# Performance work log

Hardware: AMD Instinct MI355X
Metric: run time of the kernel (lower is better)

The kernel has to match this reference:

```python
import jax, jax.numpy as jnp
import numpy as np

B, S, H = 8, 1024, 768      # batch, seq_len, encoder hidden
T, D = 9, 64                # output_type_size, att_dim
NEG = -1e12                 # masked_fill value from original code


def rope_tables(seq_len, dim):
    # theta_i = 10000^(-2i/dim), repeat_interleave(2) -> [t0,t0,t1,t1,...]
    pos = jnp.arange(seq_len, dtype=jnp.float32)[:, None]           # [S,1]
    theta = jnp.power(10000.0, -2.0 * jnp.arange(dim // 2, dtype=jnp.float32) / dim)
    theta = jnp.repeat(theta, 2)                                     # [D]
    ang = pos * theta[None, :]                                       # [S,D]
    return jnp.cos(ang), jnp.sin(ang)


def setup_inputs() -> dict:
    key = jax.random.key(0)
    k1, k2 = jax.random.split(key)
    hidden = jax.random.normal(k1, (B, S, H), dtype=jnp.float32)
    attention_mask = jnp.ones((B, S), dtype=jnp.int32)
    # xavier_normal-ish init for dense weight [2*T*D, H], zero bias
    fan = H + T * D * 2
    W = jax.random.normal(k2, (T * D * 2, H), dtype=jnp.float32) * (2.0 / fan) ** 0.5
    b = jnp.zeros((T * D * 2,), dtype=jnp.float32)
    return {"hidden": hidden, "attention_mask": attention_mask, "W": W, "b": b}


def reference(hidden, attention_mask, W, b):
    Bsz, Sl, _ = hidden.shape
    out = hidden @ W.T + b                          # [B,S,2*T*D]
    out = out.reshape(Bsz, Sl, T, D, 2)
    q = out[..., 0].transpose(0, 2, 1, 3)           # [B,T,S,D]
    k = out[..., 1].transpose(0, 2, 1, 3)           # [B,T,S,D]

    cos, sin = rope_tables(Sl, D)                   # [S,D] each

    def rot(x):
        # faithful to original: cat([-x[...,1::2], x[...,::2]], -1), NOT interleaved
        x2 = jnp.concatenate([-x[..., 1::2], x[..., ::2]], axis=-1)
        return x * cos + x2 * sin

    q, k = rot(q), rot(k)

    logits = jnp.einsum('btmd,btnd->btmn', q, k)    # [B,T,S,S]

    am = attention_mask.astype(bool)
    pad = am[:, None, :, None] & am[:, None, None, :]   # [B,1,S,S]
    triu = jnp.triu(jnp.ones((Sl, Sl), dtype=bool))     # spans i<=j
    return jnp.where(pad & triu, logits, NEG)
```

## Files before the change

kernel.cpp:

```cpp
#include <hip/hip_runtime.h>

#define S_LEN 1024
#define HID   768
#define T_SZ  9
#define NEG_VAL (-1e12f)

typedef __bf16 bf16x8 __attribute__((ext_vector_type(8)));
typedef float  f32x4  __attribute__((ext_vector_type(4)));
typedef short  short8 __attribute__((ext_vector_type(8)));
typedef short  short4v __attribute__((ext_vector_type(4)));
typedef float  float4v __attribute__((ext_vector_type(4)));

__device__ __forceinline__ unsigned short f2bf(float f) {
    unsigned int u = __builtin_bit_cast(unsigned int, f);
    u += 0x7FFFu + ((u >> 16) & 1u);
    return (unsigned short)(u >> 16);
}

__device__ __forceinline__ void gload_lds16(const void* g, void* l) {
    __builtin_amdgcn_global_load_lds(
        (const __attribute__((address_space(1))) unsigned int*)g,
        (__attribute__((address_space(3))) unsigned int*)l,
        16, 0, 0);
}

__global__ __launch_bounds__(256) void k_convert(const float* __restrict__ src,
                                                 unsigned short* __restrict__ dst,
                                                 int n8) {
    int i = blockIdx.x * 256 + threadIdx.x;
    if (i >= n8) return;
    float4v a = *((const float4v*)src + (size_t)i * 2);
    float4v b = *((const float4v*)src + (size_t)i * 2 + 1);
    short8 o;
    o[0] = (short)f2bf(a[0]); o[1] = (short)f2bf(a[1]);
    o[2] = (short)f2bf(a[2]); o[3] = (short)f2bf(a[3]);
    o[4] = (short)f2bf(b[0]); o[5] = (short)f2bf(b[1]);
    o[6] = (short)f2bf(b[2]); o[7] = (short)f2bf(b[3]);
    *(short8*)(dst + (size_t)i * 8) = o;
}

__global__ void k_tables(float* __restrict__ cosT, float* __restrict__ sinT) {
    int idx = blockIdx.x * 256 + threadIdx.x;
    int s = idx >> 6;
    int d = idx & 63;
    float theta = exp2f(-13.2877123795f * (float)(d >> 1) * (1.0f / 32.0f));
    float ang = (float)s * theta;
    float sv, cv;
    sincosf(ang, &sv, &cv);
    cosT[idx] = cv;
    sinT[idx] = sv;
}

__global__ __launch_bounds__(256) void k_proj_rope(
    const unsigned short* __restrict__ hidB,
    const unsigned short* __restrict__ wB,
    const float* __restrict__ bias,
    const float* __restrict__ cosT,
    const float* __restrict__ sinT,
    unsigned short* __restrict__ qout,
    unsigned short* __restrict__ kout)
{
    __shared__ union __align__(16) {
        struct { unsigned short A[128 * 64]; unsigned short B[128 * 64]; } st;
        unsigned short Tr[128 * 136];
    } sm;

    int tid = threadIdx.x;
    int mt = blockIdx.x / 9;
    int t  = blockIdx.x % 9;
    int m0 = mt * 128;
    int n0 = t * 128;

    int lane = tid & 63;
    int wave = tid >> 6;
    int lr = lane & 15;
    int lq = lane >> 4;
    int wrow = wave * 32;

    float bv[8];
    #pragma unroll
    for (int fn = 0; fn < 8; ++fn) bv[fn] = bias[n0 + fn * 16 + lr];

    const unsigned short* aSrc[4];
    const unsigned short* bSrc[4];
    #pragma unroll
    for (int it = 0; it < 4; ++it) {
        int gsi = (wave * 4 + it) * 64 + lane;
        int r = gsi >> 3;
        int sw = gsi & 7;
        int seg8 = (sw ^ (r & 7)) << 3;
        aSrc[it] = hidB + (size_t)(m0 + r) * HID + seg8;
        bSrc[it] = wB  + (size_t)(n0 + r) * HID + seg8;
    }

    f32x4 acc[2][8];
    #pragma unroll
    for (int i = 0; i < 2; ++i)
        #pragma unroll
        for (int j = 0; j < 8; ++j) acc[i][j] = (f32x4){0.f, 0.f, 0.f, 0.f};

    for (int kk = 0; kk < HID / 64; ++kk) {
        __syncthreads();
        #pragma unroll
        for (int it = 0; it < 4; ++it) {
            gload_lds16(aSrc[it] + kk * 64, &sm.st.A[(wave * 4 + it) * 512]);
            gload_lds16(bSrc[it] + kk * 64, &sm.st.B[(wave * 4 + it) * 512]);
        }
        __syncthreads();
        #pragma unroll
        for (int kb = 0; kb < 2; ++kb) {
            bf16x8 af[2];
            #pragma unroll
            for (int fm = 0; fm < 2; ++fm) {
                int r = wrow + fm * 16 + lr;
                int seg = kb * 4 + lq;
                af[fm] = *(const bf16x8*)&sm.st.A[r * 64 + ((seg ^ (r & 7)) * 8)];
            }
            #pragma unroll
            for (int fn = 0; fn < 8; ++fn) {
                int r = fn * 16 + lr;
                int seg = kb * 4 + lq;
                bf16x8 bfr = *(const bf16x8*)&sm.st.B[r * 64 + ((seg ^ (r & 7)) * 8)];
                acc[0][fn] = __builtin_amdgcn_mfma_f32_16x16x32_bf16(af[0], bfr, acc[0][fn], 0, 0, 0);
                acc[1][fn] = __builtin_amdgcn_mfma_f32_16x16x32_bf16(af[1], bfr, acc[1][fn], 0, 0, 0);
            }
        }
    }
    __syncthreads();

    #pragma unroll
    for (int fm = 0; fm < 2; ++fm) {
        #pragma unroll
        for (int fn = 0; fn < 8; ++fn) {
            int col = fn * 16 + lr;
            int r0 = wrow + fm * 16 + lq * 4;
            short4v pk;
            #pragma unroll
            for (int j = 0; j < 4; ++j) pk[j] = (short)f2bf(acc[fm][fn][j] + bv[fn]);
            *(short4v*)&sm.Tr[col * 136 + r0] = pk;
        }
    }
    __syncthreads();

    int d = tid & 63;
    int grp = tid >> 6;
    int cq = 2 * d, ck = 2 * d + 1;
    int pq = (d < 32) ? (4 * d + 2) : (4 * (d - 32));
    int pk2 = pq + 1;
    float sgn = (d < 32) ? -1.0f : 1.0f;
    #pragma unroll
    for (int ch = 0; ch < 4; ++ch) {
        int r0 = grp * 32 + ch * 8;
        bf16x8 xq = *(const bf16x8*)&sm.Tr[cq * 136 + r0];
        bf16x8 xk = *(const bf16x8*)&sm.Tr[ck * 136 + r0];
        bf16x8 yq = *(const bf16x8*)&sm.Tr[pq * 136 + r0];
        bf16x8 yk = *(const bf16x8*)&sm.Tr[pk2 * 136 + r0];
        #pragma unroll
        for (int rr = 0; rr < 8; ++rr) {
            int gm = m0 + r0 + rr;
            int s  = gm & (S_LEN - 1);
            int bb = gm >> 10;
            float cv = cosT[s * 64 + d];
            float sv = sinT[s * 64 + d];
            float qv = (float)xq[rr] * cv + sgn * (float)yq[rr] * sv;
            float kv = (float)xk[rr] * cv + sgn * (float)yk[rr] * sv;
            size_t ob = (((size_t)bb * T_SZ + t) * S_LEN + s) * 64 + d;
            qout[ob] = f2bf(qv);
            kout[ob] = f2bf(kv);
        }
    }
}

__global__ __launch_bounds__(256) void k_logits(
    const unsigned short* __restrict__ q,
    const unsigned short* __restrict__ k,
    const int* __restrict__ mask,
    float* __restrict__ out)
{
    int tid = threadIdx.x;
    int bt  = blockIdx.x >> 6;
    int rem = blockIdx.x & 63;
    int ti = rem >> 3;
    int tj = rem & 7;
    size_t obase = ((size_t)bt * S_LEN + (size_t)ti * 128) * S_LEN + tj * 128;

    if (ti > tj) {
        float4v nv = {NEG_VAL, NEG_VAL, NEG_VAL, NEG_VAL};
        #pragma unroll
        for (int it = 0; it < 16; ++it) {
            int idx = it * 256 + tid;
            int r = idx >> 5;
            int c4 = idx & 31;
            __builtin_nontemporal_store(nv, (float4v*)&out[obase + (size_t)r * S_LEN + c4 * 4]);
        }
        return;
    }

    __shared__ __align__(16) unsigned short As[128 * 64];
    __shared__ __align__(16) unsigned short Bs[128 * 64];
    __shared__ int mi[128], mj[128];

    int b = bt / 9;
    if (tid < 128) mi[tid] = mask[b * S_LEN + ti * 128 + tid];
    else           mj[tid - 128] = mask[b * S_LEN + tj * 128 + (tid - 128)];

    const unsigned short* qsrc = q + ((size_t)bt * S_LEN + (size_t)ti * 128) * 64;
    const unsigned short* ksrc = k + ((size_t)bt * S_LEN + (size_t)tj * 128) * 64;

    int lane = tid & 63;
    int wave = tid >> 6;
    #pragma unroll
    for (int it = 0; it < 4; ++it) {
        int gsi = (wave * 4 + it) * 64 + lane;
        int r = gsi >> 3;
        int sw = gsi & 7;
        int off = r * 64 + ((sw ^ (r & 7)) << 3);
        gload_lds16(qsrc + off, &As[(wave * 4 + it) * 512]);
        gload_lds16(ksrc + off, &Bs[(wave * 4 + it) * 512]);
    }
    __syncthreads();

    int lr = lane & 15;
    int lq = lane >> 4;
    int wrow = wave * 32;

    f32x4 acc[2][8];
    #pragma unroll
    for (int i = 0; i < 2; ++i)
        #pragma unroll
        for (int j = 0; j < 8; ++j) acc[i][j] = (f32x4){0.f, 0.f, 0.f, 0.f};

    #pragma unroll
    for (int kb = 0; kb < 2; ++kb) {
        bf16x8 qf[2];
        #pragma unroll
        for (int fi = 0; fi < 2; ++fi) {
            int r = wrow + fi * 16 + lr;
            int seg = kb * 4 + lq;
            qf[fi] = *(const bf16x8*)&As[r * 64 + ((seg ^ (r & 7)) * 8)];
        }
        #pragma unroll
        for (int fn = 0; fn < 8; ++fn) {
            int r = fn * 16 + lr;
            int seg = kb * 4 + lq;
            bf16x8 kf = *(const bf16x8*)&Bs[r * 64 + ((seg ^ (r & 7)) * 8)];
            acc[0][fn] = __builtin_amdgcn_mfma_f32_16x16x32_bf16(kf, qf[0], acc[0][fn], 0, 0, 0);
            acc[1][fn] = __builtin_amdgcn_mfma_f32_16x16x32_bf16(kf, qf[1], acc[1][fn], 0, 0, 0);
        }
    }

    #pragma unroll
    for (int fi = 0; fi < 2; ++fi) {
        int il = wrow + fi * 16 + lr;
        int gi = ti * 128 + il;
        bool mrow = mi[il] != 0;
        size_t rbase = obase + (size_t)il * S_LEN;
        #pragma unroll
        for (int fn = 0; fn < 8; ++fn) {
            int j0 = fn * 16 + lq * 4;
            int gj0 = tj * 128 + j0;
            float4v v;
            #pragma unroll
            for (int e = 0; e < 4; ++e) {
                bool ok = mrow && (mj[j0 + e] != 0) && (gi <= gj0 + e);
                v[e] = ok ? acc[fi][fn][e] : NEG_VAL;
            }
            __builtin_nontemporal_store(v, (float4v*)&out[rbase + j0]);
        }
    }
}

extern "C" void kernel_launch(void* const* d_in, const int* in_sizes, int n_in,
                              void* d_out, int out_size, void* d_ws, size_t ws_size,
                              hipStream_t stream) {
    const float* hidden = (const float*)d_in[0];
    const int*   mask   = (const int*)d_in[1];
    const float* W      = (const float*)d_in[2];
    const float* bias   = (const float*)d_in[3];
    float* out = (float*)d_out;
    int Bsz = in_sizes[0] / (S_LEN * HID);

    char* ws = (char*)d_ws;
    float* cosT = (float*)ws;
    float* sinT = (float*)(ws + (size_t)S_LEN * 64 * 4);
    unsigned short* hidB = (unsigned short*)(ws + 2ull * S_LEN * 64 * 4);
    size_t hidElems = (size_t)Bsz * S_LEN * HID;
    unsigned short* wB = hidB + hidElems;
    size_t wElems = (size_t)2 * T_SZ * 64 * HID;
    unsigned short* qb = wB + wElems;
    size_t qkElems = (size_t)Bsz * T_SZ * S_LEN * 64;
    unsigned short* kb = qb + qkElems;

    int n8h = (int)(hidElems / 8);
    int n8w = (int)(wElems / 8);
    k_convert<<<dim3((n8h + 255) / 256), dim3(256), 0, stream>>>(hidden, hidB, n8h);
    k_convert<<<dim3((n8w + 255) / 256), dim3(256), 0, stream>>>(W, wB, n8w);
    k_tables<<<dim3(S_LEN * 64 / 256), dim3(256), 0, stream>>>(cosT, sinT);
    k_proj_rope<<<dim3(Bsz * 8 * 9), dim3(256), 0, stream>>>(hidB, wB, bias, cosT, sinT, qb, kb);
    k_logits<<<dim3(Bsz * T_SZ * 64), dim3(256), 0, stream>>>(qb, kb, mask, out);
}
```

Measured before the change: 378.6 us.

## Fuse all stages into one cooperative persistent kernel with grid syncs

Replaces the five separate launches with a single cooperative kernel of 1024 workgroups. Grid-wide syncs separate the convert/table, projection and logits phases. Workgroups left idle during projection write the masked lower-triangle fill tiles, overlapping those stores with the GEMM, and tile indices are remapped to spread work. This removes launch gaps and the idle tail between kernels, at the cost of grid-sync overhead and occupancy limits from the 1024-block cooperative grid. If the cooperative launch fails, it falls back to the original multi-kernel path.

```diff
diff --git a/kernel.cpp b/kernel.cpp
--- a/kernel.cpp
+++ b/kernel.cpp
@@ -1,9 +1,13 @@
 #include <hip/hip_runtime.h>
+#include <hip/hip_cooperative_groups.h>
+
+namespace cg = cooperative_groups;
 
 #define S_LEN 1024
 #define HID   768
 #define T_SZ  9
 #define NEG_VAL (-1e12f)
+#define NWG   1024
 
 typedef __bf16 bf16x8 __attribute__((ext_vector_type(8)));
 typedef float  f32x4  __attribute__((ext_vector_type(4)));
@@ -24,11 +28,16 @@
         16, 0, 0);
 }
 
-__global__ __launch_bounds__(256) void k_convert(const float* __restrict__ src,
-                                                 unsigned short* __restrict__ dst,
-                                                 int n8) {
-    int i = blockIdx.x * 256 + threadIdx.x;
-    if (i >= n8) return;
+union __align__(16) SmU {
+    struct { unsigned short A[128 * 64]; unsigned short B[128 * 64]; } st;
+    unsigned short Tr[128 * 136];
+    struct { unsigned short As[128 * 64]; unsigned short Bs[128 * 64];
+             int mi[128]; int mj[128]; } lg;
+};
+
+
+__device__ __forceinline__ void do_convert(const float* __restrict__ src,
+                                           unsigned short* __restrict__ dst, int i) {
     float4v a = *((const float4v*)src + (size_t)i * 2);
     float4v b = *((const float4v*)src + (size_t)i * 2 + 1);
     short8 o;
@@ -39,8 +48,7 @@
     *(short8*)(dst + (size_t)i * 8) = o;
 }
 
-__global__ void k_tables(float* __restrict__ cosT, float* __restrict__ sinT) {
-    int idx = blockIdx.x * 256 + threadIdx.x;
+__device__ __forceinline__ void do_table(float* __restrict__ cosT, float* __restrict__ sinT, int idx) {
     int s = idx >> 6;
     int d = idx & 63;
     float theta = exp2f(-13.2877123795f * (float)(d >> 1) * (1.0f / 32.0f));
@@ -51,23 +59,13 @@
     sinT[idx] = sv;
 }
 
-__global__ __launch_bounds__(256) void k_proj_rope(
-    const unsigned short* __restrict__ hidB,
-    const unsigned short* __restrict__ wB,
-    const float* __restrict__ bias,
-    const float* __restrict__ cosT,
-    const float* __restrict__ sinT,
-    unsigned short* __restrict__ qout,
-    unsigned short* __restrict__ kout)
-{
-    __shared__ union __align__(16) {
-        struct { unsigned short A[128 * 64]; unsigned short B[128 * 64]; } st;
-        unsigned short Tr[128 * 136];
-    } sm;
-
+__device__ __forceinline__ void proj_tile(
+    SmU& sm, int mt, int t,
+    const unsigned short* __restrict__ hidB, const unsigned short* __restrict__ wB,
+    const float* __restrict__ bias, const float* __restrict__ cosT, const float* __restrict__ sinT,
+    unsigned short* __restrict__ qout, unsigned short* __restrict__ kout)
+{
     int tid = threadIdx.x;
-    int mt = blockIdx.x / 9;
-    int t  = blockIdx.x % 9;
     int m0 = mt * 128;
     int n0 = t * 128;
 
@@ -169,40 +167,31 @@
             kout[ob] = f2bf(kv);
         }
     }
-}
-
-__global__ __launch_bounds__(256) void k_logits(
-    const unsigned short* __restrict__ q,
-    const unsigned short* __restrict__ k,
-    const int* __restrict__ mask,
-    float* __restrict__ out)
+    __syncthreads();
+}
+
+__device__ __forceinline__ void fill_tile(float* __restrict__ out, int bt, int ti, int tj) {
+    size_t obase = ((size_t)bt * S_LEN + (size_t)ti * 128) * S_LEN + tj * 128;
+    float4v nv = {NEG_VAL, NEG_VAL, NEG_VAL, NEG_VAL};
+    #pragma unroll
+    for (int it = 0; it < 16; ++it) {
+        int idx = it * 256 + threadIdx.x;
+        int r = idx >> 5;
+        int c4 = idx & 31;
+        __builtin_nontemporal_store(nv, (float4v*)&out[obase + (size_t)r * S_LEN + c4 * 4]);
+    }
+}
+
+__device__ __forceinline__ void logits_tile(
+    SmU& sm, const unsigned short* __restrict__ q, const unsigned short* __restrict__ k,
+    const int* __restrict__ mask, float* __restrict__ out, int Bsz, int bt, int ti, int tj)
 {
     int tid = threadIdx.x;
-    int bt  = blockIdx.x >> 6;
-    int rem = blockIdx.x & 63;
-    int ti = rem >> 3;
-    int tj = rem & 7;
     size_t obase = ((size_t)bt * S_LEN + (size_t)ti * 128) * S_LEN + tj * 128;
 
-    if (ti > tj) {
-        float4v nv = {NEG_VAL, NEG_VAL, NEG_VAL, NEG_VAL};
-        #pragma unroll
-        for (int it = 0; it < 16; ++it) {
-            int idx = it * 256 + tid;
-            int r = idx >> 5;
-            int c4 = idx & 31;
-            __builtin_nontemporal_store(nv, (float4v*)&out[obase + (size_t)r * S_LEN + c4 * 4]);
-        }
-        return;
-    }
-
-    __shared__ __align__(16) unsigned short As[128 * 64];
-    __shared__ __align__(16) unsigned short Bs[128 * 64];
-    __shared__ int mi[128], mj[128];
-
-    int b = bt / 9;
-    if (tid < 128) mi[tid] = mask[b * S_LEN + ti * 128 + tid];
-    else           mj[tid - 128] = mask[b * S_LEN + tj * 128 + (tid - 128)];
+    int b = bt / T_SZ;
+    if (tid < 128) sm.lg.mi[tid] = mask[b * S_LEN + ti * 128 + tid];
+    else           sm.lg.mj[tid - 128] = mask[b * S_LEN + tj * 128 + (tid - 128)];
 
     const unsigned short* qsrc = q + ((size_t)bt * S_LEN + (size_t)ti * 128) * 64;
     const unsigned short* ksrc = k + ((size_t)bt * S_LEN + (size_t)tj * 128) * 64;
@@ -215,8 +204,8 @@
         int r = gsi >> 3;
         int sw = gsi & 7;
         int off = r * 64 + ((sw ^ (r & 7)) << 3);
-        gload_lds16(qsrc + off, &As[(wave * 4 + it) * 512]);
-        gload_lds16(ksrc + off, &Bs[(wave * 4 + it) * 512]);
+        gload_lds16(qsrc + off, &sm.lg.As[(wave * 4 + it) * 512]);
+        gload_lds16(ksrc + off, &sm.lg.Bs[(wave * 4 + it) * 512]);
     }
     __syncthreads();
 
@@ -237,13 +226,13 @@
         for (int fi = 0; fi < 2; ++fi) {
             int r = wrow + fi * 16 + lr;
             int seg = kb * 4 + lq;
-            qf[fi] = *(const bf16x8*)&As[r * 64 + ((seg ^ (r & 7)) * 8)];
+            qf[fi] = *(const bf16x8*)&sm.lg.As[r * 64 + ((seg ^ (r & 7)) * 8)];
         }
         #pragma unroll
         for (int fn = 0; fn < 8; ++fn) {
             int r = fn * 16 + lr;
             int seg = kb * 4 + lq;
-            bf16x8 kf = *(const bf16x8*)&Bs[r * 64 + ((seg ^ (r & 7)) * 8)];
+            bf16x8 kf = *(const bf16x8*)&sm.lg.Bs[r * 64 + ((seg ^ (r & 7)) * 8)];
             acc[0][fn] = __builtin_amdgcn_mfma_f32_16x16x32_bf16(kf, qf[0], acc[0][fn], 0, 0, 0);
             acc[1][fn] = __builtin_amdgcn_mfma_f32_16x16x32_bf16(kf, qf[1], acc[1][fn], 0, 0, 0);
         }
@@ -253,7 +242,7 @@
     for (int fi = 0; fi < 2; ++fi) {
         int il = wrow + fi * 16 + lr;
         int gi = ti * 128 + il;
-        bool mrow = mi[il] != 0;
+        bool mrow = sm.lg.mi[il] != 0;
         size_t rbase = obase + (size_t)il * S_LEN;
         #pragma unroll
         for (int fn = 0; fn < 8; ++fn) {
@@ -262,12 +251,95 @@
             float4v v;
             #pragma unroll
             for (int e = 0; e < 4; ++e) {
-                bool ok = mrow && (mj[j0 + e] != 0) && (gi <= gj0 + e);
+                bool ok = mrow && (sm.lg.mj[j0 + e] != 0) && (gi <= gj0 + e);
                 v[e] = ok ? acc[fi][fn][e] : NEG_VAL;
             }
             __builtin_nontemporal_store(v, (float4v*)&out[rbase + j0]);
         }
     }
+    __syncthreads();
+}
+
+__global__ __launch_bounds__(256, 4) void mega(
+    const float* __restrict__ hidden, const int* __restrict__ mask,
+    const float* __restrict__ W, const float* __restrict__ bias,
+    float* __restrict__ out, float* cosT, float* sinT,
+    unsigned short* hidB, unsigned short* wB,
+    unsigned short* qb, unsigned short* kb,
+    int Bsz, int n8h, int n8w)
+{
+    __shared__ SmU sm;
+    cg::grid_group grid = cg::this_grid();
+
+    int gtid = blockIdx.x * 256 + threadIdx.x;
+    int gs   = gridDim.x * 256;
+    for (int i = gtid; i < n8h; i += gs) do_convert(hidden, hidB, i);
+    for (int i = gtid; i < n8w; i += gs) do_convert(W, wB, i);
+    for (int i = gtid; i < S_LEN * 64; i += gs) do_table(cosT, sinT, i);
+    grid.sync();
+
+    int nproj = Bsz * 72;
+    for (int b2 = blockIdx.x; b2 < nproj; b2 += gridDim.x) {
+        int tile = (b2 & 7) * (nproj >> 3) + (b2 >> 3);
+        proj_tile(sm, tile / T_SZ, tile % T_SZ, hidB, wB, bias, cosT, sinT, qb, kb);
+    }
+    {
+        int nf = Bsz * T_SZ * 28;
+        int fillStart, fillStride;
+        if (nproj < (int)gridDim.x) { fillStart = (int)blockIdx.x - nproj; fillStride = (int)gridDim.x - nproj; }
+        else                        { fillStart = (int)blockIdx.x;          fillStride = (int)gridDim.x; }
+        if (fillStart >= 0)
+            for (int f = fillStart; f < nf; f += fillStride) {
+                int bt = f / 28, rr = f % 28;
+                int ti = 1; while (rr >= ti) { rr -= ti; ++ti; }
+                fill_tile(out, bt, ti, rr);
+            }
+    }
+    grid.sync();
+
+    int ncomp = Bsz * T_SZ * 36;
+    int cc = ncomp >> 3;
+    for (int x = blockIdx.x; x < ncomp; x += gridDim.x) {
+        int c = ((ncomp & 7) == 0) ? ((x & 7) * cc + (x >> 3)) : x;
+        int bt = c / 36, r = c % 36;
+        int ti = 0; while (r >= 8 - ti) { r -= 8 - ti; ++ti; }
+        logits_tile(sm, qb, kb, mask, out, Bsz, bt, ti, ti + r);
+    }
+}
+
+__global__ __launch_bounds__(256) void k_convert_fb(const float* __restrict__ src,
+                                                    unsigned short* __restrict__ dst, int n8) {
+    int i = blockIdx.x * 256 + threadIdx.x;
+    if (i < n8) do_convert(src, dst, i);
+}
+
+__global__ void k_tables_fb(float* cosT, float* sinT) {
+    do_table(cosT, sinT, blockIdx.x * 256 + threadIdx.x);
+}
+
+__global__ __launch_bounds__(256) void k_proj_fb(
+    const unsigned short* __restrict__ hidB, const unsigned short* __restrict__ wB,
+    const float* __restrict__ bias, const float* __restrict__ cosT, const float* __restrict__ sinT,
+    unsigned short* __restrict__ qb, unsigned short* __restrict__ kb)
+{
+    __shared__ SmU sm;
+    int npj = gridDim.x;
+    int b = blockIdx.x;
+    int tile = ((npj & 7) == 0) ? ((b & 7) * (npj >> 3) + (b >> 3)) : b;
+    proj_tile(sm, tile / T_SZ, tile % T_SZ, hidB, wB, bias, cosT, sinT, qb, kb);
+}
+
+__global__ __launch_bounds__(256) void k_logits_fb(
+    const unsigned short* __restrict__ q, const unsigned short* __restrict__ k,
+    const int* __restrict__ mask, float* __restrict__ out, int Bsz)
+{
+    __shared__ SmU sm;
+    int bt  = blockIdx.x >> 6;
+    int rem = blockIdx.x & 63;
+    int ti = rem >> 3;
+    int tj = rem & 7;
+    if (ti > tj) fill_tile(out, bt, ti, tj);
+    else         logits_tile(sm, q, k, mask, out, Bsz, bt, ti, tj);
 }
 
 extern "C" void kernel_launch(void* const* d_in, const int* in_sizes, int n_in,
@@ -293,9 +365,18 @@
 
     int n8h = (int)(hidElems / 8);
     int n8w = (int)(wElems / 8);
-    k_convert<<<dim3((n8h + 255) / 256), dim3(256), 0, stream>>>(hidden, hidB, n8h);
-    k_convert<<<dim3((n8w + 255) / 256), dim3(256), 0, stream>>>(W, wB, n8w);
-    k_tables<<<dim3(S_LEN * 64 / 256), dim3(256), 0, stream>>>(cosT, sinT);
-    k_proj_rope<<<dim3(Bsz * 8 * 9), dim3(256), 0, stream>>>(hidB, wB, bias, cosT, sinT, qb, kb);
-    k_logits<<<dim3(Bsz * T_SZ * 64), dim3(256), 0, stream>>>(qb, kb, mask, out);
-}
+
+    void* args[] = { (void*)&hidden, (void*)&mask, (void*)&W, (void*)&bias,
+                     (void*)&out, (void*)&cosT, (void*)&sinT,
+                     (void*)&hidB, (void*)&wB, (void*)&qb, (void*)&kb,
+                     (void*)&Bsz, (void*)&n8h, (void*)&n8w };
+    hipError_t err = hipLaunchCooperativeKernel((const void*)mega, dim3(NWG), dim3(256),
+                                                args, 0, stream);
+    if (err != hipSuccess) {
+        k_convert_fb<<<dim3((n8h + 255) / 256), dim3(256), 0, stream>>>(hidden, hidB, n8h);
+        k_convert_fb<<<dim3((n8w + 255) / 256), dim3(256), 0, stream>>>(W, wB, n8w);
+        k_tables_fb<<<dim3(S_LEN * 64 / 256), dim3(256), 0, stream>>>(cosT, sinT);
+        k_proj_fb<<<dim3(Bsz * 72), dim3(256), 0, stream>>>(hidB, wB, bias, cosT, sinT, qb, kb);
+        k_logits_fb<<<dim3(Bsz * T_SZ * 64), dim3(256), 0, stream>>>(qb, kb, mask, out, Bsz);
+    }
+}
```

Result: slower. 626.1 us (+65.4%).

## Merge prep kernels, double-buffer projection GEMM, overlap masked fill with projection

Applied to the files above, without the earlier changes.

Merges the two convert launches and the rope table launch into one prep kernel. Double-buffers the LDS tiles in the projection GEMM so the load of the next K slice overlaps MFMA work, with one barrier per iteration instead of two. Moves the lower-triangle NEG fill blocks out of the logits kernel into the projection launch so that store-heavy work runs alongside the GEMM, and the logits grid now only covers upper-triangle tiles. Doubling LDS use in the projection kernel may reduce occupancy.

```diff
diff --git a/kernel.cpp b/kernel.cpp
--- a/kernel.cpp
+++ b/kernel.cpp
@@ -24,11 +24,8 @@
         16, 0, 0);
 }
 
-__global__ __launch_bounds__(256) void k_convert(const float* __restrict__ src,
-                                                 unsigned short* __restrict__ dst,
-                                                 int n8) {
-    int i = blockIdx.x * 256 + threadIdx.x;
-    if (i >= n8) return;
+__device__ __forceinline__ void do_convert(const float* __restrict__ src,
+                                           unsigned short* __restrict__ dst, int i) {
     float4v a = *((const float4v*)src + (size_t)i * 2);
     float4v b = *((const float4v*)src + (size_t)i * 2 + 1);
     short8 o;
@@ -39,35 +36,65 @@
     *(short8*)(dst + (size_t)i * 8) = o;
 }
 
-__global__ void k_tables(float* __restrict__ cosT, float* __restrict__ sinT) {
-    int idx = blockIdx.x * 256 + threadIdx.x;
-    int s = idx >> 6;
-    int d = idx & 63;
-    float theta = exp2f(-13.2877123795f * (float)(d >> 1) * (1.0f / 32.0f));
-    float ang = (float)s * theta;
-    float sv, cv;
-    sincosf(ang, &sv, &cv);
-    cosT[idx] = cv;
-    sinT[idx] = sv;
-}
-
-__global__ __launch_bounds__(256) void k_proj_rope(
+__global__ __launch_bounds__(256) void k_prep(
+    const float* __restrict__ hidden, const float* __restrict__ W,
+    unsigned short* __restrict__ hidB, unsigned short* __restrict__ wB,
+    float* __restrict__ cosT, float* __restrict__ sinT, int n8h, int n8w)
+{
+    int i = blockIdx.x * 256 + threadIdx.x;
+    if (i < n8h) { do_convert(hidden, hidB, i); return; }
+    i -= n8h;
+    if (i < n8w) { do_convert(W, wB, i); return; }
+    i -= n8w;
+    if (i < S_LEN * 64) {
+        int s = i >> 6;
+        int d = i & 63;
+        float theta = exp2f(-13.2877123795f * (float)(d >> 1) * (1.0f / 32.0f));
+        float ang = (float)s * theta;
+        float sv, cv;
+        sincosf(ang, &sv, &cv);
+        cosT[i] = cv;
+        sinT[i] = sv;
+    }
+}
+
+union __align__(16) SmP {
+    unsigned short buf[2][2][128 * 64];
+    unsigned short Tr[128 * 136];
+};
+
+__global__ __launch_bounds__(256) void k_proj_fill(
     const unsigned short* __restrict__ hidB,
     const unsigned short* __restrict__ wB,
     const float* __restrict__ bias,
     const float* __restrict__ cosT,
     const float* __restrict__ sinT,
     unsigned short* __restrict__ qout,
-    unsigned short* __restrict__ kout)
+    unsigned short* __restrict__ kout,
+    float* __restrict__ out, int nproj)
 {
-    __shared__ union __align__(16) {
-        struct { unsigned short A[128 * 64]; unsigned short B[128 * 64]; } st;
-        unsigned short Tr[128 * 136];
-    } sm;
-
+    __shared__ SmP sm;
     int tid = threadIdx.x;
-    int mt = blockIdx.x / 9;
-    int t  = blockIdx.x % 9;
+    int blk = blockIdx.x;
+
+    if (blk >= nproj) {
+        int f = blk - nproj;
+        int bt = f / 28, rr = f % 28;
+        int ti = 1; while (rr >= ti) { rr -= ti; ++ti; }
+        size_t obase = ((size_t)bt * S_LEN + (size_t)ti * 128) * S_LEN + rr * 128;
+        float4v nv = {NEG_VAL, NEG_VAL, NEG_VAL, NEG_VAL};
+        #pragma unroll
+        for (int it = 0; it < 16; ++it) {
+            int idx = it * 256 + tid;
+            int r = idx >> 5;
+            int c4 = idx & 31;
+            __builtin_nontemporal_store(nv, (float4v*)&out[obase + (size_t)r * S_LEN + c4 * 4]);
+        }
+        return;
+    }
+
+    int mt = blk / T_SZ;
+    int t  = blk % T_SZ;
     int m0 = mt * 128;
     int n0 = t * 128;
 
@@ -99,14 +126,22 @@
         #pragma unroll
         for (int j = 0; j < 8; ++j) acc[i][j] = (f32x4){0.f, 0.f, 0.f, 0.f};
 
+    #pragma unroll
+    for (int it = 0; it < 4; ++it) {
+        gload_lds16(aSrc[it], &sm.buf[0][0][(wave * 4 + it) * 512]);
+        gload_lds16(bSrc[it], &sm.buf[0][1][(wave * 4 + it) * 512]);
+    }
+    __syncthreads();
+
     for (int kk = 0; kk < HID / 64; ++kk) {
-        __syncthreads();
-        #pragma unroll
-        for (int it = 0; it < 4; ++it) {
-            gload_lds16(aSrc[it] + kk * 64, &sm.st.A[(wave * 4 + it) * 512]);
-            gload_lds16(bSrc[it] + kk * 64, &sm.st.B[(wave * 4 + it) * 512]);
-        }
-        __syncthreads();
+        int par = kk & 1;
+        if (kk < HID / 64 - 1) {
+            #pragma unroll
+            for (int it = 0; it < 4; ++it) {
+                gload_lds16(aSrc[it] + (kk + 1) * 64, &sm.buf[par ^ 1][0][(wave * 4 + it) * 512]);
+                gload_lds16(bSrc[it] + (kk + 1) * 64, &sm.buf[par ^ 1][1][(wave * 4 + it) * 512]);
+            }
+        }
         #pragma unroll
         for (int kb = 0; kb < 2; ++kb) {
             bf16x8 af[2];
@@ -114,19 +149,19 @@
             for (int fm = 0; fm < 2; ++fm) {
                 int r = wrow + fm * 16 + lr;
                 int seg = kb * 4 + lq;
-                af[fm] = *(const bf16x8*)&sm.st.A[r * 64 + ((seg ^ (r & 7)) * 8)];
+                af[fm] = *(const bf16x8*)&sm.buf[par][0][r * 64 + ((seg ^ (r & 7)) * 8)];
             }
             #pragma unroll
             for (int fn = 0; fn < 8; ++fn) {
                 int r = fn * 16 + lr;
                 int seg = kb * 4 + lq;
-                bf16x8 bfr = *(const bf16x8*)&sm.st.B[r * 64 + ((seg ^ (r & 7)) * 8)];
+                bf16x8 bfr = *(const bf16x8*)&sm.buf[par][1][r * 64 + ((seg ^ (r & 7)) * 8)];
                 acc[0][fn] = __builtin_amdgcn_mfma_f32_16x16x32_bf16(af[0], bfr, acc[0][fn], 0, 0, 0);
                 acc[1][fn] = __builtin_amdgcn_mfma_f32_16x16x32_bf16(af[1], bfr, acc[1][fn], 0, 0, 0);
             }
         }
-    }
-    __syncthreads();
+        __syncthreads();
+    }
 
     #pragma unroll
     for (int fm = 0; fm < 2; ++fm) {
@@ -177,30 +212,18 @@
     const int* __restrict__ mask,
     float* __restrict__ out)
 {
-    int tid = threadIdx.x;
-    int bt  = blockIdx.x >> 6;
-    int rem = blockIdx.x & 63;
-    int ti = rem >> 3;
-    int tj = rem & 7;
-    size_t obase = ((size_t)bt * S_LEN + (size_t)ti * 128) * S_LEN + tj * 128;
-
-    if (ti > tj) {
-        float4v nv = {NEG_VAL, NEG_VAL, NEG_VAL, NEG_VAL};
-        #pragma unroll
-        for (int it = 0; it < 16; ++it) {
-            int idx = it * 256 + tid;
-            int r = idx >> 5;
-            int c4 = idx & 31;
-            __builtin_nontemporal_store(nv, (float4v*)&out[obase + (size_t)r * S_LEN + c4 * 4]);
-        }
-        return;
-    }
-
     __shared__ __align__(16) unsigned short As[128 * 64];
     __shared__ __align__(16) unsigned short Bs[128 * 64];
     __shared__ int mi[128], mj[128];
 
-    int b = bt / 9;
+    int tid = threadIdx.x;
+    int c = blockIdx.x;
+    int bt = c / 36, r = c % 36;
+    int ti = 0; while (r >= 8 - ti) { r -= 8 - ti; ++ti; }
+    int tj = ti + r;
+    size_t obase = ((size_t)bt * S_LEN + (size_t)ti * 128) * S_LEN + tj * 128;
+
+    int b = bt / T_SZ;
     if (tid < 128) mi[tid] = mask[b * S_LEN + ti * 128 + tid];
     else           mj[tid - 128] = mask[b * S_LEN + tj * 128 + (tid - 128)];
 
@@ -212,9 +235,9 @@
     #pragma unroll
     for (int it = 0; it < 4; ++it) {
         int gsi = (wave * 4 + it) * 64 + lane;
-        int r = gsi >> 3;
+        int rr = gsi >> 3;
         int sw = gsi & 7;
-        int off = r * 64 + ((sw ^ (r & 7)) << 3);
+        int off = rr * 64 + ((sw ^ (rr & 7)) << 3);
         gload_lds16(qsrc + off, &As[(wave * 4 + it) * 512]);
         gload_lds16(ksrc + off, &Bs[(wave * 4 + it) * 512]);
     }
@@ -235,15 +258,15 @@
         bf16x8 qf[2];
         #pragma unroll
         for (int fi = 0; fi < 2; ++fi) {
-            int r = wrow + fi * 16 + lr;
+            int rr = wrow + fi * 16 + lr;
             int seg = kb * 4 + lq;
-            qf[fi] = *(const bf16x8*)&As[r * 64 + ((seg ^ (r & 7)) * 8)];
+            qf[fi] = *(const bf16x8*)&As[rr * 64 + ((seg ^ (rr & 7)) * 8)];
         }
         #pragma unroll
         for (int fn = 0; fn < 8; ++fn) {
-            int r = fn * 16 + lr;
+            int rr = fn * 16 + lr;
             int seg = kb * 4 + lq;
-            bf16x8 kf = *(const bf16x8*)&Bs[r * 64 + ((seg ^ (r & 7)) * 8)];
+            bf16x8 kf = *(const bf16x8*)&Bs[rr * 64 + ((seg ^ (rr & 7)) * 8)];
             acc[0][fn] = __builtin_amdgcn_mfma_f32_16x16x32_bf16(kf, qf[0], acc[0][fn], 0, 0, 0);
             acc[1][fn] = __builtin_amdgcn_mfma_f32_16x16x32_bf16(kf, qf[1], acc[1][fn], 0, 0, 0);
         }
@@ -293,9 +316,13 @@
 
     int n8h = (int)(hidElems / 8);
     int n8w = (int)(wElems / 8);
-    k_convert<<<dim3((n8h + 255) / 256), dim3(256), 0, stream>>>(hidden, hidB, n8h);
-    k_convert<<<dim3((n8w + 255) / 256), dim3(256), 0, stream>>>(W, wB, n8w);
-    k_tables<<<dim3(S_LEN * 64 / 256), dim3(256), 0, stream>>>(cosT, sinT);
-    k_proj_rope<<<dim3(Bsz * 8 * 9), dim3(256), 0, stream>>>(hidB, wB, bias, cosT, sinT, qb, kb);
-    k_logits<<<dim3(Bsz * T_SZ * 64), dim3(256), 0, stream>>>(qb, kb, mask, out);
-}
+    int nPrep = (n8h + n8w + S_LEN * 64 + 255) / 256;
+    int nproj = Bsz * 72;
+    int nfill = Bsz * T_SZ * 28;
+    int ncomp = Bsz * T_SZ * 36;
+
+    k_prep<<<dim3(nPrep), dim3(256), 0, stream>>>(hidden, W, hidB, wB, cosT, sinT, n8h, n8w);
+    k_proj_fill<<<dim3(nproj + nfill), dim3(256), 0, stream>>>(hidB, wB, bias, cosT, sinT,
+                                                               qb, kb, out, nproj);
+    k_logits<<<dim3(ncomp), dim3(256), 0, stream>>>(qb, kb, mask, out);
+}
```

Result: no change. 381.7 us (+0.8%).
